# Performance work log

Measured on AMD Instinct MI355X. Metric: run time of the kernel, lower is better.

Reference implementation:

```python
import jax, jax.numpy as jnp
import numpy as np

NEG_SLOPE = 0.01  # F.leaky_relu default
BN_EPS = 1e-5


def _nnconv_bn_lrelu(x, src, dst, ef, W_edge, b_edge, W_root, b_root, gamma, beta):
    # PyG NNConv (aggr='add'): msg_e = x_src[e] @ reshape(nn(edge_feat[e]), [in, out])
    E = ef.shape[0]
    in_c = x.shape[1]
    out_c = W_root.shape[1]
    We = (ef @ W_edge.T + b_edge).reshape(E, in_c, out_c)   # [E, in, out]
    msg = jnp.einsum('ei,eio->eo', x[src], We)               # gather + per-edge matvec
    aggr = jax.ops.segment_sum(msg, dst, num_segments=x.shape[0])  # scatter-add
    h = aggr + x @ W_root + b_root
    # BatchNorm1d in training mode: batch statistics over nodes (biased var)
    mean = jnp.mean(h, axis=0)
    var = jnp.var(h, axis=0)
    hn = (h - mean) * jax.lax.rsqrt(var + BN_EPS) * gamma + beta
    return jnp.where(hn > 0, hn, NEG_SLOPE * hn)             # LeakyReLU


def setup_inputs() -> dict:
    key = jax.random.key(0)
    ks = jax.random.split(key, 12)
    N, E = 8192, 32768
    D_NODE, D_EDGE, H, OUT = 64, 64, 64, 128
    node_features = jax.random.normal(ks[0], (N, D_NODE), dtype=jnp.float32)
    edge_index = jax.random.randint(ks[1], (2, E), 0, N, dtype=jnp.int32)
    edge_features = jax.random.normal(ks[2], (E, D_EDGE), dtype=jnp.float32)
    batch = jnp.zeros((N,), dtype=jnp.int32)
    s = 0.05
    params = {
        # layer 0: node_feats=D_NODE, edge_feats=D_EDGE, out=H
        'W_edge0': jax.random.normal(ks[3], (D_NODE * H, D_EDGE), dtype=jnp.float32) * s,
        'b_edge0': jnp.zeros((D_NODE * H,), dtype=jnp.float32),
        'W_root0': jax.random.normal(ks[4], (D_NODE, H), dtype=jnp.float32) * s,
        'b_root0': jnp.zeros((H,), dtype=jnp.float32),
        'gamma0': jnp.ones((H,), dtype=jnp.float32),
        'beta0': jnp.zeros((H,), dtype=jnp.float32),
        # layer 1: node_feats=H, edge_feats=H(==D_EDGE), out=H
        'W_edge1': jax.random.normal(ks[5], (H * H, D_EDGE), dtype=jnp.float32) * s,
        'b_edge1': jnp.zeros((H * H,), dtype=jnp.float32),
        'W_root1': jax.random.normal(ks[6], (H, H), dtype=jnp.float32) * s,
        'b_root1': jnp.zeros((H,), dtype=jnp.float32),
        'gamma1': jnp.ones((H,), dtype=jnp.float32),
        'beta1': jnp.zeros((H,), dtype=jnp.float32),
        # final linear
        'W_lin': jax.random.normal(ks[7], (OUT, H), dtype=jnp.float32) * s,
        'b_lin': jnp.zeros((OUT,), dtype=jnp.float32),
    }
    return {'node_features': node_features, 'edge_index': edge_index,
            'edge_features': edge_features, 'batch': batch, **params}


def reference(node_features, edge_index, edge_features, batch,
              W_edge0, b_edge0, W_root0, b_root0, gamma0, beta0,
              W_edge1, b_edge1, W_root1, b_root1, gamma1, beta1,
              W_lin, b_lin):
    src, dst = edge_index[0], edge_index[1]
    h = _nnconv_bn_lrelu(node_features, src, dst, edge_features,
                         W_edge0, b_edge0, W_root0, b_root0, gamma0, beta0)
    h = _nnconv_bn_lrelu(h, src, dst, edge_features,
                         W_edge1, b_edge1, W_root1, b_root1, gamma1, beta1)
    # dropout treated as identity (eval-mode determinism)
    return h @ W_lin.T + b_lin
```

## Files before the change

kernel.cpp:

```cpp
#include <hip/hip_runtime.h>

typedef __bf16 bf16x8 __attribute__((ext_vector_type(8)));
typedef float f32x4 __attribute__((ext_vector_type(4)));

#define NEG_SLOPE 0.01f
#define BN_EPS 1e-5f

static __device__ __forceinline__ unsigned short f2bf(float f) {
    unsigned u = __builtin_bit_cast(unsigned, f);
    unsigned r = (u + 0x7fffu + ((u >> 16) & 1u)) >> 16;
    return (unsigned short)r;
}
static __device__ __forceinline__ float lrelu(float v) {
    return fmaxf(v, 0.f) + NEG_SLOPE * fminf(v, 0.f);
}
static __device__ __forceinline__ f32x4 bn4(f32x4 v, f32x4 sc, f32x4 sh) {
    f32x4 r = v * sc + sh;
    r.x = lrelu(r.x); r.y = lrelu(r.y); r.z = lrelu(r.z); r.w = lrelu(r.w);
    return r;
}

__global__ __launch_bounds__(256) void prep(const float* __restrict__ We0,
                                            const float* __restrict__ We1,
                                            unsigned short* __restrict__ wbs0,
                                            unsigned short* __restrict__ wbs1,
                                            float* __restrict__ stats,
                                            int* __restrict__ counters,
                                            const int* __restrict__ dst,
                                            int* __restrict__ hist, int E) {
    const int idx = blockIdx.x * 256 + threadIdx.x;
    if (blockIdx.x == 0) {
        stats[threadIdx.x] = 0.f;
        if (threadIdx.x < 2) counters[threadIdx.x] = 0;
    }
    if (idx < 65536) {
        const int t = idx;
        const float* We = (t >> 15) ? We1 : We0;
        unsigned short* wbs = (t >> 15) ? wbs1 : wbs0;
        const int r = t & 32767;
        const int i = r >> 9, os = (r >> 7) & 3, h = (r >> 6) & 1, l = r & 63;
        const float* sp = We + (size_t)(i * 64 + 16 * os + (l & 15)) * 64
                             + h * 32 + 8 * (l >> 4);
        const f32x4 v0 = *reinterpret_cast<const f32x4*>(sp);
        const f32x4 v1 = *reinterpret_cast<const f32x4*>(sp + 4);
        ushort4 u0, u1;
        u0.x = f2bf(v0.x); u0.y = f2bf(v0.y); u0.z = f2bf(v0.z); u0.w = f2bf(v0.w);
        u1.x = f2bf(v1.x); u1.y = f2bf(v1.y); u1.z = f2bf(v1.z); u1.w = f2bf(v1.w);
        *reinterpret_cast<ushort4*>(wbs + (size_t)r * 8) = u0;
        *reinterpret_cast<ushort4*>(wbs + (size_t)r * 8 + 4) = u1;
    } else {
        const int e = idx - 65536;
        if (e < E) atomicAdd(&hist[dst[e]], 1);
    }
}

__global__ __launch_bounds__(256) void scan_kernel(const int* __restrict__ hist,
                                                   int* __restrict__ ofs,
                                                   int* __restrict__ cur, int N) {
    __shared__ int wsum[4];
    const int tid = threadIdx.x;
    const int per = N / 256;
    const int base = tid * per;
    int loc[32];
    int s = 0;
#pragma unroll
    for (int k = 0; k < 32; ++k) { loc[k] = s; s += hist[base + k]; }
    const int lane = tid & 63, w = tid >> 6;
    int run = s;
#pragma unroll
    for (int d = 1; d < 64; d <<= 1) {
        int up = __shfl_up(run, d, 64);
        if (lane >= d) run += up;
    }
    const int excl = run - s;
    if (lane == 63) wsum[w] = run;
    __syncthreads();
    int woff = 0;
#pragma unroll
    for (int i = 0; i < 4; ++i) woff += (i < w) ? wsum[i] : 0;
    if (tid == 255) ofs[N] = woff + run;
    const int off = woff + excl;
#pragma unroll
    for (int k = 0; k < 32; ++k) {
        ofs[base + k] = off + loc[k];
        cur[base + k] = off + loc[k];
    }
}

__global__ __launch_bounds__(256) void scatter_kernel(const int* __restrict__ dst,
                                                      int* __restrict__ cur,
                                                      int* __restrict__ perm) {
    const int e = blockIdx.x * 256 + threadIdx.x;
    perm[e] = atomicAdd(&cur[dst[e]], 1);
}

__global__ __launch_bounds__(256) void reorder_ef(const float* __restrict__ ef,
                                                  const int* __restrict__ perm,
                                                  const int* __restrict__ src,
                                                  unsigned short* __restrict__ ef_bs,
                                                  int* __restrict__ src_s) {
    const int idx = blockIdx.x * 256 + threadIdx.x;
    const int e = idx >> 4, c = idx & 15;
    const int p = perm[e];
    const f32x4 v = *reinterpret_cast<const f32x4*>(ef + (size_t)e * 64 + c * 4);
    ushort4 u;
    u.x = f2bf(v.x); u.y = f2bf(v.y); u.z = f2bf(v.z); u.w = f2bf(v.w);
    *reinterpret_cast<ushort4*>(ef_bs + (size_t)p * 64 + c * 4) = u;
    if (c == 0) src_s[p] = src[e];
}

__global__ __launch_bounds__(256) void node_mm2(const float* __restrict__ x,
                                                const float* __restrict__ Wr,
                                                const float* __restrict__ br,
                                                float* __restrict__ aggr,
                                                const float* __restrict__ be,
                                                float* __restrict__ NB,
                                                const float* __restrict__ ss) {
    const float* M; const float* bias; float* out;
    if (blockIdx.y == 0) { M = Wr; bias = br; out = aggr; }
    else                 { M = be; bias = nullptr; out = NB; }
    __shared__ float Ml[64][64];
    __shared__ float xl[64][64];
    const int tid = threadIdx.x;
    const int n0 = blockIdx.x * 64;
    for (int f = tid; f < 1024; f += 256) {
        int r = f >> 4, c = f & 15;
        *reinterpret_cast<float4*>(&Ml[r][c * 4]) =
            *reinterpret_cast<const float4*>(M + (size_t)r * 64 + c * 4);
        f32x4 xv = *reinterpret_cast<const f32x4*>(x + (size_t)(n0 + r) * 64 + c * 4);
        if (ss) {
            const f32x4 sc = *reinterpret_cast<const f32x4*>(ss + c * 4);
            const f32x4 sh = *reinterpret_cast<const f32x4*>(ss + 64 + c * 4);
            xv = bn4(xv, sc, sh);
        }
        *reinterpret_cast<f32x4*>(&xl[r][c * 4]) = xv;
    }
    __syncthreads();
    const int o = tid & 63, g = tid >> 6;
    float acc[16] = {};
    for (int i4 = 0; i4 < 16; ++i4) {
        float m0 = Ml[4 * i4 + 0][o], m1 = Ml[4 * i4 + 1][o];
        float m2 = Ml[4 * i4 + 2][o], m3 = Ml[4 * i4 + 3][o];
#pragma unroll
        for (int k = 0; k < 16; ++k) {
            const f32x4 xv = *reinterpret_cast<const f32x4*>(&xl[g + 4 * k][4 * i4]);
            acc[k] += xv.x * m0 + xv.y * m1 + xv.z * m2 + xv.w * m3;
        }
    }
    const float b = bias ? bias[o] : 0.f;
#pragma unroll
    for (int k = 0; k < 16; ++k)
        out[(size_t)(n0 + g + 4 * k) * 64 + o] = acc[k] + b;
}

__global__ __launch_bounds__(512, 2) void msg_fused(
    const unsigned short* __restrict__ ef_bs,
    const unsigned short* __restrict__ wbs,
    const float* __restrict__ x,
    const float* __restrict__ NB,
    const int* __restrict__ src_s,
    float* __restrict__ msg,
    const float* __restrict__ ss) {
    __shared__ unsigned short wlds[16384];
    __shared__ float xT2[8192];
    const int tid = threadIdx.x;
    const int e0 = blockIdx.x * 128;

#pragma unroll
    for (int it = 0; it < 4; ++it) {
        int f = it * 512 + tid;
        int e = f & 127, c = f >> 7;
        int s = src_s[e0 + e];
        f32x4 xv = *reinterpret_cast<const f32x4*>(x + (size_t)s * 64 + c * 4);
        if (ss) {
            const f32x4 sc = *reinterpret_cast<const f32x4*>(ss + c * 4);
            const f32x4 sh = *reinterpret_cast<const f32x4*>(ss + 64 + c * 4);
            xv = bn4(xv, sc, sh);
        }
        const int eln = e & 15, ehh = e >> 4;
        xT2[(4 * c + 0) * 128 + eln * 8 + ehh] = xv.x;
        xT2[(4 * c + 1) * 128 + eln * 8 + ehh] = xv.y;
        xT2[(4 * c + 2) * 128 + eln * 8 + ehh] = xv.z;
        xT2[(4 * c + 3) * 128 + eln * 8 + ehh] = xv.w;
    }

    const int w = tid >> 6, l = tid & 63, lg = l >> 4, ln = l & 15;
    const int os = w & 3, eh = w >> 2;

    bf16x8 B0[4], B1[4];
#pragma unroll
    for (int tt = 0; tt < 4; ++tt) {
        const unsigned short* pe = ef_bs + (size_t)(e0 + 64 * eh + 16 * tt + ln) * 64 + 8 * lg;
        B0[tt] = *reinterpret_cast<const bf16x8*>(pe);
        B1[tt] = *reinterpret_cast<const bf16x8*>(pe + 32);
    }

    const char* gW = (const char*)wbs;
    char* wldsB = (char*)wlds;
#define GLD(c, j) (*reinterpret_cast<const bf16x8*>(gW + (size_t)(c) * 32768 + (j) * 8192 + tid * 16))
#define SST(j, v) (*reinterpret_cast<bf16x8*>(wldsB + (j) * 8192 + tid * 16) = (v))

    bf16x8 S0 = GLD(0, 0), S1 = GLD(0, 1), S2 = GLD(0, 2), S3 = GLD(0, 3);
    SST(0, S0); SST(1, S1); SST(2, S2); SST(3, S3);
    S0 = GLD(1, 0); S1 = GLD(1, 1); S2 = GLD(1, 2); S3 = GLD(1, 3);
    __syncthreads();

    f32x4 acc[4] = {};
    const unsigned short* wb_ = wlds + os * 1024 + l * 8;
    for (int t = 0; t < 16; ++t) {
#pragma unroll
        for (int ii = 0; ii < 4; ++ii) {
            const bf16x8 A0 = *reinterpret_cast<const bf16x8*>(wb_ + ii * 4096);
            const bf16x8 A1 = *reinterpret_cast<const bf16x8*>(wb_ + ii * 4096 + 512);
            const f32x4 xs = *reinterpret_cast<const f32x4*>(
                &xT2[(t * 4 + ii) * 128 + ln * 8 + eh * 4]);
#pragma unroll
            for (int tt = 0; tt < 4; ++tt) {
                f32x4 c = {};
                c = __builtin_amdgcn_mfma_f32_16x16x32_bf16(A0, B0[tt], c, 0, 0, 0);
                c = __builtin_amdgcn_mfma_f32_16x16x32_bf16(A1, B1[tt], c, 0, 0, 0);
                acc[tt] += xs[tt] * c;
            }
        }
        __syncthreads();
        if (t < 15) {
            SST(0, S0); SST(1, S1); SST(2, S2); SST(3, S3);
            if (t < 14) {
                S0 = GLD(t + 2, 0); S1 = GLD(t + 2, 1);
                S2 = GLD(t + 2, 2); S3 = GLD(t + 2, 3);
            }
            __syncthreads();
        }
    }
#undef GLD
#undef SST

#pragma unroll
    for (int tt = 0; tt < 4; ++tt) {
        const int e = e0 + 64 * eh + 16 * tt + ln;
        const int s = src_s[e];
        const f32x4 nbv = *reinterpret_cast<const f32x4*>(NB + (size_t)s * 64 + os * 16 + 4 * lg);
        const f32x4 add = acc[tt] + nbv;
        *reinterpret_cast<f32x4*>(msg + (size_t)e * 64 + os * 16 + 4 * lg) = add;
    }
}

__global__ __launch_bounds__(256) void gather_k(const float* __restrict__ msg,
                                                const int* __restrict__ ofs,
                                                float* __restrict__ aggr) {
    const int tid = threadIdx.x;
    const int w = tid >> 6, lane = tid & 63;
    const int v = blockIdx.x * 4 + w;
    const int beg = ofs[v], end = ofs[v + 1];
    float a0 = 0.f, a1 = 0.f, a2 = 0.f, a3 = 0.f;
    int j = beg;
    for (; j + 4 <= end; j += 4) {
        a0 += msg[(size_t)(j + 0) * 64 + lane];
        a1 += msg[(size_t)(j + 1) * 64 + lane];
        a2 += msg[(size_t)(j + 2) * 64 + lane];
        a3 += msg[(size_t)(j + 3) * 64 + lane];
    }
    for (; j < end; ++j) a0 += msg[(size_t)j * 64 + lane];
    aggr[(size_t)v * 64 + lane] += (a0 + a1) + (a2 + a3);
}

__global__ __launch_bounds__(256) void bn_stats(const float* __restrict__ h,
                                                float* __restrict__ sums,
                                                const float* __restrict__ gamma,
                                                const float* __restrict__ beta,
                                                float* __restrict__ ss,
                                                float invN,
                                                int* __restrict__ counter,
                                                int nblk) {
    const int tid = threadIdx.x;
    const int o = tid & 63, g = tid >> 6;
    const int n0 = blockIdx.x * 128;
    float s = 0.f, s2 = 0.f;
    for (int k = 0; k < 32; ++k) {
        float v = h[(size_t)(n0 + g * 32 + k) * 64 + o];
        s += v; s2 += v * v;
    }
    __shared__ float red[2][4][64];
    __shared__ int lastFlag;
    red[0][g][o] = s; red[1][g][o] = s2;
    __syncthreads();
    if (g == 0) {
        s  = red[0][0][o] + red[0][1][o] + red[0][2][o] + red[0][3][o];
        s2 = red[1][0][o] + red[1][1][o] + red[1][2][o] + red[1][3][o];
        atomicAdd(&sums[o], s);
        atomicAdd(&sums[64 + o], s2);
    }
    __threadfence();
    __syncthreads();
    if (tid == 0) lastFlag = (atomicAdd(counter, 1) == nblk - 1);
    __syncthreads();
    if (lastFlag && tid < 64) {
        const float sv  = atomicAdd(&sums[tid], 0.f);
        const float sv2 = atomicAdd(&sums[64 + tid], 0.f);
        const float mean = sv * invN;
        const float var  = sv2 * invN - mean * mean;
        const float sc = gamma[tid] * rsqrtf(var + BN_EPS);
        ss[tid] = sc;
        ss[64 + tid] = beta[tid] - mean * sc;
    }
}

__global__ __launch_bounds__(256) void out_kernel(const float* __restrict__ x2,
                                                  const float* __restrict__ Wl,
                                                  const float* __restrict__ bl,
                                                  float* __restrict__ out,
                                                  const float* __restrict__ ss) {
    __shared__ float Wt[64][129];
    __shared__ float xl[64][64];
    const int tid = threadIdx.x;
    const int n0 = blockIdx.x * 64;
    for (int f = tid; f < 8192; f += 256) {
        int q = f >> 6, o = f & 63;
        Wt[o][q] = Wl[f];
    }
    for (int f = tid; f < 1024; f += 256) {
        int r = f >> 4, c = f & 15;
        f32x4 xv = *reinterpret_cast<const f32x4*>(x2 + (size_t)(n0 + r) * 64 + c * 4);
        const f32x4 sc = *reinterpret_cast<const f32x4*>(ss + c * 4);
        const f32x4 sh = *reinterpret_cast<const f32x4*>(ss + 64 + c * 4);
        xv = bn4(xv, sc, sh);
        *reinterpret_cast<f32x4*>(&xl[r][c * 4]) = xv;
    }
    __syncthreads();
    const int q = tid & 127, ng = tid >> 7;
    float acc[32] = {};
    for (int o4 = 0; o4 < 16; ++o4) {
        float w0 = Wt[4 * o4 + 0][q], w1 = Wt[4 * o4 + 1][q];
        float w2 = Wt[4 * o4 + 2][q], w3 = Wt[4 * o4 + 3][q];
#pragma unroll
        for (int k = 0; k < 32; ++k) {
            const f32x4 xv = *reinterpret_cast<const f32x4*>(&xl[ng + 2 * k][4 * o4]);
            acc[k] += xv.x * w0 + xv.y * w1 + xv.z * w2 + xv.w * w3;
        }
    }
    const float b = bl[q];
#pragma unroll
    for (int k = 0; k < 32; ++k)
        out[(size_t)(n0 + ng + 2 * k) * 128 + q] = acc[k] + b;
}

extern "C" void kernel_launch(void* const* d_in, const int* in_sizes, int n_in,
                              void* d_out, int out_size, void* d_ws, size_t ws_size,
                              hipStream_t stream) {
    const float* nf      = (const float*)d_in[0];
    const int*   ei      = (const int*)d_in[1];
    const float* ef      = (const float*)d_in[2];
    const float* W_edge0 = (const float*)d_in[4];
    const float* b_edge0 = (const float*)d_in[5];
    const float* W_root0 = (const float*)d_in[6];
    const float* b_root0 = (const float*)d_in[7];
    const float* gamma0  = (const float*)d_in[8];
    const float* beta0   = (const float*)d_in[9];
    const float* W_edge1 = (const float*)d_in[10];
    const float* b_edge1 = (const float*)d_in[11];
    const float* W_root1 = (const float*)d_in[12];
    const float* b_root1 = (const float*)d_in[13];
    const float* gamma1  = (const float*)d_in[14];
    const float* beta1   = (const float*)d_in[15];
    const float* W_lin   = (const float*)d_in[16];
    const float* b_lin   = (const float*)d_in[17];

    const int N = in_sizes[0] / 64;
    const int E = in_sizes[1] / 2;
    const int* src = ei;
    const int* dst = ei + E;

    unsigned short* ef_bs = (unsigned short*)d_ws;
    unsigned short* wbs0  = ef_bs + (size_t)E * 64;
    unsigned short* wbs1  = wbs0 + 262144;
    float* msg   = (float*)(wbs1 + 262144);
    float* aggr0 = msg + (size_t)E * 64;
    float* aggr1 = aggr0 + (size_t)N * 64;
    float* NBbuf = aggr1 + (size_t)N * 64;
    float* stats = NBbuf + (size_t)N * 64;
    float* ssbuf = stats + 256;
    int*   cnt   = (int*)(ssbuf + 256);
    int*   hist  = cnt + 2;
    int*   ofs   = hist + N;
    int*   cur   = ofs + N + 1;
    int*   perm  = cur + N;
    int*   src_s = perm + E;

    const float invN = 1.0f / (float)N;

    hipMemsetAsync(hist, 0, N * sizeof(int), stream);
    prep<<<(65536 + E) / 256, 256, 0, stream>>>(W_edge0, W_edge1, wbs0, wbs1,
                                                stats, cnt, dst, hist, E);
    scan_kernel<<<1, 256, 0, stream>>>(hist, ofs, cur, N);
    scatter_kernel<<<E / 256, 256, 0, stream>>>(dst, cur, perm);
    reorder_ef<<<E * 16 / 256, 256, 0, stream>>>(ef, perm, src, ef_bs, src_s);

    node_mm2<<<dim3(N / 64, 2), 256, 0, stream>>>(nf, W_root0, b_root0, aggr0,
                                                  b_edge0, NBbuf, nullptr);
    msg_fused<<<E / 128, 512, 0, stream>>>(ef_bs, wbs0, nf, NBbuf, src_s, msg, nullptr);
    gather_k<<<N / 4, 256, 0, stream>>>(msg, ofs, aggr0);
    bn_stats<<<N / 128, 256, 0, stream>>>(aggr0, stats, gamma0, beta0, ssbuf,
                                          invN, cnt + 0, N / 128);

    node_mm2<<<dim3(N / 64, 2), 256, 0, stream>>>(aggr0, W_root1, b_root1, aggr1,
                                                  b_edge1, NBbuf, ssbuf);
    msg_fused<<<E / 128, 512, 0, stream>>>(ef_bs, wbs1, aggr0, NBbuf, src_s, msg, ssbuf);
    gather_k<<<N / 4, 256, 0, stream>>>(msg, ofs, aggr1);
    bn_stats<<<N / 128, 256, 0, stream>>>(aggr1, stats + 128, gamma1, beta1, ssbuf + 128,
                                          invN, cnt + 1, N / 128);

    out_kernel<<<N / 64, 256, 0, stream>>>(aggr1, W_lin, b_lin, (float*)d_out, ssbuf + 128);
}
```

Baseline: 143.8 us.

## Fuse edge scatter with feature reorder and double weight tile per stage in msg kernel

Merges the atomic scatter and the edge-feature reorder into one kernel, so each thread takes its slot and writes the bf16 row itself, dropping the perm buffer and one launch. In msg_fused, each LDS weight stage now holds twice as many input rows (64KB), so the loop runs 8 iterations with 8 sub-steps instead of 16 with 4. That halves the barrier and staging rounds. The larger LDS footprint and launch_bounds(512,1) cut occupancy to one block per CU, and the fused scatter does uncoalesced per-thread row reads and writes.

```diff
diff --git a/kernel.cpp b/kernel.cpp
--- a/kernel.cpp
+++ b/kernel.cpp
@@ -87,26 +87,22 @@
     }
 }
 
-__global__ __launch_bounds__(256) void scatter_kernel(const int* __restrict__ dst,
-                                                      int* __restrict__ cur,
-                                                      int* __restrict__ perm) {
+__global__ __launch_bounds__(256) void scatter_reorder(
+    const int* __restrict__ dst, const int* __restrict__ src,
+    const float* __restrict__ ef, int* __restrict__ cur,
+    unsigned short* __restrict__ ef_bs, int* __restrict__ src_s) {
     const int e = blockIdx.x * 256 + threadIdx.x;
-    perm[e] = atomicAdd(&cur[dst[e]], 1);
-}
-
-__global__ __launch_bounds__(256) void reorder_ef(const float* __restrict__ ef,
-                                                  const int* __restrict__ perm,
-                                                  const int* __restrict__ src,
-                                                  unsigned short* __restrict__ ef_bs,
-                                                  int* __restrict__ src_s) {
-    const int idx = blockIdx.x * 256 + threadIdx.x;
-    const int e = idx >> 4, c = idx & 15;
-    const int p = perm[e];
-    const f32x4 v = *reinterpret_cast<const f32x4*>(ef + (size_t)e * 64 + c * 4);
-    ushort4 u;
-    u.x = f2bf(v.x); u.y = f2bf(v.y); u.z = f2bf(v.z); u.w = f2bf(v.w);
-    *reinterpret_cast<ushort4*>(ef_bs + (size_t)p * 64 + c * 4) = u;
-    if (c == 0) src_s[p] = src[e];
+    const int p = atomicAdd(&cur[dst[e]], 1);
+    src_s[p] = src[e];
+    const float* er = ef + (size_t)e * 64;
+    unsigned short* orow = ef_bs + (size_t)p * 64;
+#pragma unroll
+    for (int c = 0; c < 16; ++c) {
+        const f32x4 v = *reinterpret_cast<const f32x4*>(er + 4 * c);
+        ushort4 u;
+        u.x = f2bf(v.x); u.y = f2bf(v.y); u.z = f2bf(v.z); u.w = f2bf(v.w);
+        *reinterpret_cast<ushort4*>(orow + 4 * c) = u;
+    }
 }
 
 __global__ __launch_bounds__(256) void node_mm2(const float* __restrict__ x,
@@ -153,7 +149,7 @@
         out[(size_t)(n0 + g + 4 * k) * 64 + o] = acc[k] + b;
 }
 
-__global__ __launch_bounds__(512, 2) void msg_fused(
+__global__ __launch_bounds__(512, 1) void msg_fused(
     const unsigned short* __restrict__ ef_bs,
     const unsigned short* __restrict__ wbs,
     const float* __restrict__ x,
@@ -161,7 +157,7 @@
     const int* __restrict__ src_s,
     float* __restrict__ msg,
     const float* __restrict__ ss) {
-    __shared__ unsigned short wlds[16384];
+    __shared__ unsigned short wlds[32768];
     __shared__ float xT2[8192];
     const int tid = threadIdx.x;
     const int e0 = blockIdx.x * 128;
@@ -197,23 +193,26 @@
 
     const char* gW = (const char*)wbs;
     char* wldsB = (char*)wlds;
-#define GLD(c, j) (*reinterpret_cast<const bf16x8*>(gW + (size_t)(c) * 32768 + (j) * 8192 + tid * 16))
+#define GLD(c, j) (*reinterpret_cast<const bf16x8*>(gW + (size_t)(c) * 65536 + (j) * 8192 + tid * 16))
 #define SST(j, v) (*reinterpret_cast<bf16x8*>(wldsB + (j) * 8192 + tid * 16) = (v))
 
     bf16x8 S0 = GLD(0, 0), S1 = GLD(0, 1), S2 = GLD(0, 2), S3 = GLD(0, 3);
+    bf16x8 S4 = GLD(0, 4), S5 = GLD(0, 5), S6 = GLD(0, 6), S7 = GLD(0, 7);
     SST(0, S0); SST(1, S1); SST(2, S2); SST(3, S3);
+    SST(4, S4); SST(5, S5); SST(6, S6); SST(7, S7);
     S0 = GLD(1, 0); S1 = GLD(1, 1); S2 = GLD(1, 2); S3 = GLD(1, 3);
+    S4 = GLD(1, 4); S5 = GLD(1, 5); S6 = GLD(1, 6); S7 = GLD(1, 7);
     __syncthreads();
 
     f32x4 acc[4] = {};
     const unsigned short* wb_ = wlds + os * 1024 + l * 8;
-    for (int t = 0; t < 16; ++t) {
-#pragma unroll
-        for (int ii = 0; ii < 4; ++ii) {
+    for (int t = 0; t < 8; ++t) {
+#pragma unroll
+        for (int ii = 0; ii < 8; ++ii) {
             const bf16x8 A0 = *reinterpret_cast<const bf16x8*>(wb_ + ii * 4096);
             const bf16x8 A1 = *reinterpret_cast<const bf16x8*>(wb_ + ii * 4096 + 512);
             const f32x4 xs = *reinterpret_cast<const f32x4*>(
-                &xT2[(t * 4 + ii) * 128 + ln * 8 + eh * 4]);
+                &xT2[(t * 8 + ii) * 128 + ln * 8 + eh * 4]);
 #pragma unroll
             for (int tt = 0; tt < 4; ++tt) {
                 f32x4 c = {};
@@ -223,11 +222,14 @@
             }
         }
         __syncthreads();
-        if (t < 15) {
+        if (t < 7) {
             SST(0, S0); SST(1, S1); SST(2, S2); SST(3, S3);
-            if (t < 14) {
+            SST(4, S4); SST(5, S5); SST(6, S6); SST(7, S7);
+            if (t < 6) {
                 S0 = GLD(t + 2, 0); S1 = GLD(t + 2, 1);
                 S2 = GLD(t + 2, 2); S3 = GLD(t + 2, 3);
+                S4 = GLD(t + 2, 4); S5 = GLD(t + 2, 5);
+                S6 = GLD(t + 2, 6); S7 = GLD(t + 2, 7);
             }
             __syncthreads();
         }
@@ -383,8 +385,7 @@
     int*   hist  = cnt + 2;
     int*   ofs   = hist + N;
     int*   cur   = ofs + N + 1;
-    int*   perm  = cur + N;
-    int*   src_s = perm + E;
+    int*   src_s = cur + N;
 
     const float invN = 1.0f / (float)N;
 
@@ -392,8 +393,7 @@
     prep<<<(65536 + E) / 256, 256, 0, stream>>>(W_edge0, W_edge1, wbs0, wbs1,
                                                 stats, cnt, dst, hist, E);
     scan_kernel<<<1, 256, 0, stream>>>(hist, ofs, cur, N);
-    scatter_kernel<<<E / 256, 256, 0, stream>>>(dst, cur, perm);
-    reorder_ef<<<E * 16 / 256, 256, 0, stream>>>(ef, perm, src, ef_bs, src_s);
+    scatter_reorder<<<E / 256, 256, 0, stream>>>(dst, src, ef, cur, ef_bs, src_s);
 
     node_mm2<<<dim3(N / 64, 2), 256, 0, stream>>>(nf, W_root0, b_root0, aggr0,
                                                   b_edge0, NBbuf, nullptr);
```

Result: no change. 144.5 us (+0.5%).
